# Optimization experiments

Hardware: AMD Instinct MI355X
Metric: run time of the kernel (lower is better)

The kernel has to match this reference:

```python
import jax, jax.numpy as jnp
import numpy as np

N_NODES = 10000
N_EDGES = 50000
NUM_GENES = 1000
HEADS = 8
DIMS_IN = [256, 448 * 8, 384 * 8, 256 * 8]
DIMS_OUT = [448, 384, 256, NUM_GENES]
HEADS_L = [8, 8, 8, 1]


def _leaky_relu(x):
    return jnp.where(x >= 0, x, 0.2 * x)


def gat_conv(x, src, dst, n, W, a_src, a_dst, b, heads, c):
    # W: [heads*c, f_in]; a_src/a_dst: [heads, c]; b: [heads*c]
    h = (x @ W.T).reshape(n, heads, c)                      # [N,H,C]
    al_s = jnp.einsum('nhc,hc->nh', h, a_src)               # [N,H]
    al_d = jnp.einsum('nhc,hc->nh', h, a_dst)
    e = _leaky_relu(al_s[src] + al_d[dst])                  # [E,H]
    # segment softmax over incoming edges of each dst node
    m = jax.ops.segment_max(e, dst, num_segments=n)
    e = jnp.exp(e - m[dst])
    s = jax.ops.segment_sum(e, dst, num_segments=n)
    alpha = e / (s[dst] + 1e-16)
    out = jax.ops.segment_sum(h[src] * alpha[:, :, None], dst, num_segments=n)
    return out.reshape(n, heads * c) + b


def graph_ln(x, w, b):
    # PyG LayerNorm mode='graph': normalize over all node features of the graph
    mu = x.mean()
    var = ((x - mu) ** 2).mean()
    return (x - mu) * jax.lax.rsqrt(var + 1e-5) * w + b


def setup_inputs() -> dict:
    key = jax.random.key(0)
    ks = jax.random.split(key, 32)
    inp = {
        'x': jax.random.normal(ks[0], (N_NODES, DIMS_IN[0]), dtype=jnp.float32),
        'edge_index': jax.random.randint(ks[1], (2, N_EDGES), 0, N_NODES, dtype=jnp.int32),
    }
    ki = 2
    for li in range(4):
        h, c, fin = HEADS_L[li], DIMS_OUT[li], DIMS_IN[li]
        inp[f'W{li+1}'] = jax.random.normal(ks[ki], (h * c, fin), dtype=jnp.float32) * (fin ** -0.5); ki += 1
        inp[f'a_src{li+1}'] = jax.random.normal(ks[ki], (h, c), dtype=jnp.float32) * 0.1; ki += 1
        inp[f'a_dst{li+1}'] = jax.random.normal(ks[ki], (h, c), dtype=jnp.float32) * 0.1; ki += 1
        inp[f'b{li+1}'] = jnp.zeros((h * c,), dtype=jnp.float32)
        if li < 3:
            inp[f'ln{li+1}_w'] = jnp.ones((h * c,), dtype=jnp.float32)
            inp[f'ln{li+1}_b'] = jnp.zeros((h * c,), dtype=jnp.float32)
    return inp


def reference(x, edge_index,
              W1, a_src1, a_dst1, b1, ln1_w, ln1_b,
              W2, a_src2, a_dst2, b2, ln2_w, ln2_b,
              W3, a_src3, a_dst3, b3, ln3_w, ln3_b,
              W4, a_src4, a_dst4, b4):
    n = x.shape[0]
    loops = jnp.arange(n, dtype=edge_index.dtype)
    src = jnp.concatenate([edge_index[0], loops])  # add_self_loops=True (PyG default)
    dst = jnp.concatenate([edge_index[1], loops])
    h = jax.nn.relu(gat_conv(x, src, dst, n, W1, a_src1, a_dst1, b1, 8, 448))
    h = graph_ln(h, ln1_w, ln1_b)
    h = jax.nn.relu(gat_conv(h, src, dst, n, W2, a_src2, a_dst2, b2, 8, 384))
    h = graph_ln(h, ln2_w, ln2_b)
    h = jax.nn.relu(gat_conv(h, src, dst, n, W3, a_src3, a_dst3, b3, 8, 256))
    h = graph_ln(h, ln3_w, ln3_b)
    out = gat_conv(h, src, dst, n, W4, a_src4, a_dst4, b4, 1, NUM_GENES)
    return out
```

## Files before the change

kernel.cpp:

```cpp
#include <hip/hip_runtime.h>

typedef _Float16 h8 __attribute__((ext_vector_type(8)));
typedef _Float16 h4 __attribute__((ext_vector_type(4)));
typedef __attribute__((ext_vector_type(4))) float facc4;

__device__ __forceinline__ void gload16(const void* g, void* l) {
  __builtin_amdgcn_global_load_lds((const __attribute__((address_space(1))) void*)g,
                                   (__attribute__((address_space(3))) void*)l, 16, 0, 0);
}

__global__ void f2h_k(const float* __restrict__ in, unsigned short* __restrict__ out, int n4) {
  int i = blockIdx.x * 256 + threadIdx.x;
  int stride = gridDim.x * 256;
  for (; i < n4; i += stride) {
    float4 v = ((const float4*)in)[i];
    h4 o;
    o[0] = (_Float16)v.x; o[1] = (_Float16)v.y; o[2] = (_Float16)v.z; o[3] = (_Float16)v.w;
    ((h4*)out)[i] = o;
  }
}

__global__ __launch_bounds__(512, 2) void gemm_f16(
    const unsigned short* __restrict__ A, const unsigned short* __restrict__ B,
    unsigned short* __restrict__ Hout,
    float* __restrict__ als, float* __restrict__ ald,
    const float* __restrict__ a_src, const float* __restrict__ a_dst,
    int M, int Nn, int K, int C, int H, int gx, int nwg) {
  __shared__ unsigned short lds[3 * 24576];
  const int tid = threadIdx.x, lane = tid & 63, wv = tid >> 6;

  int lin = blockIdx.x;
  int q = nwg >> 3, r = nwg & 7;
  int xcd = lin & 7, idx = lin >> 3;
  int swz = (xcd < r) ? (xcd * (q + 1) + idx) : (r * (q + 1) + (xcd - r) * q + idx);
  const int bx = swz % gx, by = swz / gx;
  const int brow = by * 256, bcol = bx * 128;
  const int wr = wv >> 1, wc = wv & 1;

  const int lr = lane >> 3;
  const int gslot = (lane & 7) ^ lr;
  const unsigned short* pa[4]; int ldsA[4];
#pragma unroll
  for (int i = 0; i < 4; ++i) {
    int rl = wv * 32 + i * 8 + lr;
    int rg = brow + rl; if (rg > M - 1) rg = M - 1;
    pa[i] = A + (size_t)rg * K + gslot * 8;
    ldsA[i] = (wv * 32 + i * 8) * 64;
  }
  const unsigned short* pb[2]; int ldsB[2];
#pragma unroll
  for (int i = 0; i < 2; ++i) {
    int rl = wv * 16 + i * 8 + lr;
    int rg = bcol + rl; if (rg > Nn - 1) rg = Nn - 1;
    pb[i] = B + (size_t)rg * K + gslot * 8;
    ldsB[i] = 16384 + (wv * 16 + i * 8) * 64;
  }

  const int ra0 = wr * 64 + (lane & 15);
  const int rb0 = wc * 64 + (lane & 15);
  const int g16 = lane >> 4;
  const int lx = lane & 7;

  facc4 acc[4][4] = {};
  const int nt = K >> 6;

  auto STAGE = [&](int kt, int buf) {
    const int bo = buf * 24576;
#pragma unroll
    for (int i = 0; i < 4; ++i) gload16(pa[i] + kt * 64, &lds[bo + ldsA[i]]);
#pragma unroll
    for (int i = 0; i < 2; ++i) gload16(pb[i] + kt * 64, &lds[bo + ldsB[i]]);
  };

  STAGE(0, 0);
  STAGE(1, 1);
  asm volatile("s_waitcnt vmcnt(6)" ::: "memory");
  __builtin_amdgcn_s_barrier();
  asm volatile("" ::: "memory");

  int cb = 0, sb = 2;
  for (int kt = 0; kt < nt; ++kt) {
    if (kt + 2 < nt) STAGE(kt + 2, sb);
    const int bo = cb * 24576;
#pragma unroll
    for (int kk = 0; kk < 2; ++kk) {
      const int slot = (kk * 4 + g16) ^ lx;
      h8 af[4], bf[4];
#pragma unroll
      for (int i = 0; i < 4; ++i) af[i] = *(const h8*)&lds[bo + (ra0 + i * 16) * 64 + slot * 8];
#pragma unroll
      for (int j = 0; j < 4; ++j) bf[j] = *(const h8*)&lds[bo + 16384 + (rb0 + j * 16) * 64 + slot * 8];
      __builtin_amdgcn_s_setprio(1);
#pragma unroll
      for (int i = 0; i < 4; ++i)
#pragma unroll
        for (int j = 0; j < 4; ++j)
          acc[i][j] = __builtin_amdgcn_mfma_f32_16x16x32_f16(af[i], bf[j], acc[i][j], 0, 0, 0);
      __builtin_amdgcn_s_setprio(0);
    }
    if (kt + 2 < nt) asm volatile("s_waitcnt vmcnt(6)" ::: "memory");
    else             asm volatile("s_waitcnt vmcnt(0)" ::: "memory");
    __builtin_amdgcn_s_barrier();
    asm volatile("" ::: "memory");
    cb = (cb == 2) ? 0 : cb + 1;
    sb = (sb == 2) ? 0 : sb + 1;
  }

  const int rbase = brow + wr * 64 + ((lane >> 4) << 2);
  const int cbase = bcol + wc * 64 + (lane & 15);

  float asv[4], adv[4];
#pragma unroll
  for (int j = 0; j < 4; ++j) {
    int col = cbase + j * 16;
    bool ok = col < Nn;
    asv[j] = ok ? a_src[col] : 0.f;
    adv[j] = ok ? a_dst[col] : 0.f;
  }
  const int hh = (bcol + wc * 64) / C;
#pragma unroll
  for (int i = 0; i < 4; ++i)
#pragma unroll
    for (int r2 = 0; r2 < 4; ++r2) {
      float s1 = 0.f, s2 = 0.f;
#pragma unroll
      for (int j = 0; j < 4; ++j) { float v = acc[i][j][r2]; s1 += v * asv[j]; s2 += v * adv[j]; }
#pragma unroll
      for (int m = 1; m < 16; m <<= 1) { s1 += __shfl_xor(s1, m); s2 += __shfl_xor(s2, m); }
      int row = rbase + i * 16 + r2;
      if ((lane & 15) == 0 && row < M) {
        atomicAdd(&als[row * H + hh], s1);
        atomicAdd(&ald[row * H + hh], s2);
      }
    }

#pragma unroll
  for (int i = 0; i < 4; ++i)
#pragma unroll
    for (int j = 0; j < 4; ++j) {
      int col = cbase + j * 16;
      if (col >= Nn) continue;
#pragma unroll
      for (int r2 = 0; r2 < 4; ++r2) {
        int row = rbase + i * 16 + r2;
        if (row < M) {
          _Float16 hv = (_Float16)acc[i][j][r2];
          Hout[(size_t)row * Nn + col] = *(unsigned short*)&hv;
        }
      }
    }
}

__global__ void count_deg_k(const int* __restrict__ ei, int* __restrict__ deg, int Ereal, int Etot) {
  int e = blockIdx.x * 256 + threadIdx.x;
  if (e >= Etot) return;
  int dst = (e < Ereal) ? ei[Ereal + e] : (e - Ereal);
  atomicAdd(&deg[dst], 1);
}

__global__ void scan_k(const int* __restrict__ deg, int* __restrict__ rowptr, int n) {
  __shared__ int sums[1024];
  int t = threadIdx.x;
  int base = t * 10;
  int loc[10]; int s = 0;
#pragma unroll
  for (int i = 0; i < 10; ++i) { int idx = base + i; int d = (idx < n) ? deg[idx] : 0; loc[i] = s; s += d; }
  sums[t] = s;
  __syncthreads();
  for (int off = 1; off < 1024; off <<= 1) {
    int add = (t >= off) ? sums[t - off] : 0;
    __syncthreads();
    sums[t] += add;
    __syncthreads();
  }
  int excl = sums[t] - s;
#pragma unroll
  for (int i = 0; i < 10; ++i) { int idx = base + i; if (idx < n) rowptr[idx] = excl + loc[i]; }
  if (t == 1023) rowptr[n] = sums[1023];
}

__global__ void scatter_k(const int* __restrict__ ei, const int* __restrict__ rowptr,
                          int* __restrict__ fill, int* __restrict__ esrc,
                          int Ereal, int Etot) {
  int e = blockIdx.x * 256 + threadIdx.x;
  if (e >= Etot) return;
  int src = (e < Ereal) ? ei[e] : (e - Ereal);
  int dst = (e < Ereal) ? ei[Ereal + e] : (e - Ereal);
  int pos = rowptr[dst] + atomicAdd(&fill[dst], 1);
  esrc[pos] = src;
}

template <int H, bool FP32OUT, bool STATS>
__global__ __launch_bounds__(256) void aggregate_k(
    const unsigned short* __restrict__ hfp,
    const float* __restrict__ als, const float* __restrict__ ald,
    const int* __restrict__ rowptr, const int* __restrict__ esrc,
    const float* __restrict__ bias, void* __restrict__ outv,
    float* __restrict__ lnsums, int C, int F) {
  const int node = blockIdx.x;
  const int tid = threadIdx.x;
  int beg = rowptr[node];
  int deg = rowptr[node + 1] - beg;
  if (deg > 128) deg = 128;
  __shared__ int   s_src[128];
  __shared__ float s_p[128][H];
  __shared__ float s_inv[H];
  float aldv[H];
#pragma unroll
  for (int h = 0; h < H; ++h) aldv[h] = ald[node * H + h];
  for (int d = tid; d < deg; d += 256) {
    int s = esrc[beg + d];
    s_src[d] = s;
#pragma unroll
    for (int h = 0; h < H; ++h) {
      float v = als[s * H + h] + aldv[h];
      s_p[d][h] = (v >= 0.f) ? v : 0.2f * v;
    }
  }
  __syncthreads();
  if (tid < H) {
    float m = -1e30f;
    for (int d = 0; d < deg; ++d) m = fmaxf(m, s_p[d][tid]);
    float s = 0.f;
    for (int d = 0; d < deg; ++d) { float p = __expf(s_p[d][tid] - m); s_p[d][tid] = p; s += p; }
    s_inv[tid] = 1.f / (s + 1e-16f);
  }
  __syncthreads();

  float s1 = 0.f, s2 = 0.f;
  const int F8 = F >> 3;
  for (int c8 = tid; c8 < F8; c8 += 256) {
    int f0 = c8 * 8;
    int h = f0 / C;
    float a[8];
    float4 b0 = *(const float4*)(bias + f0);
    float4 b1 = *(const float4*)(bias + f0 + 4);
    a[0] = b0.x; a[1] = b0.y; a[2] = b0.z; a[3] = b0.w;
    a[4] = b1.x; a[5] = b1.y; a[6] = b1.z; a[7] = b1.w;
    for (int d = 0; d < deg; ++d) {
      float al = s_p[d][h] * s_inv[h];
      h8 hv = *(const h8*)(hfp + (size_t)s_src[d] * F + f0);
#pragma unroll
      for (int j = 0; j < 8; ++j) a[j] = fmaf(al, (float)hv[j], a[j]);
    }
    size_t i = (size_t)node * F + f0;
    if (FP32OUT) {
      float4 o0 = {a[0], a[1], a[2], a[3]};
      float4 o1 = {a[4], a[5], a[6], a[7]};
      *(float4*)((float*)outv + i) = o0;
      *(float4*)((float*)outv + i + 4) = o1;
    } else {
      h8 o;
#pragma unroll
      for (int j = 0; j < 8; ++j) o[j] = (_Float16)a[j];
      *(h8*)((unsigned short*)outv + i) = o;
    }
    if (STATS) {
#pragma unroll
      for (int j = 0; j < 8; ++j) { float v = a[j] > 0.f ? a[j] : 0.f; s1 += v; s2 += v * v; }
    }
  }
  if (STATS) {
#pragma unroll
    for (int m = 32; m; m >>= 1) { s1 += __shfl_down(s1, m); s2 += __shfl_down(s2, m); }
    __shared__ float r1[4], r2[4];
    if ((tid & 63) == 0) { r1[tid >> 6] = s1; r2[tid >> 6] = s2; }
    __syncthreads();
    if (tid == 0) {
      atomicAdd(&lnsums[0], r1[0] + r1[1] + r1[2] + r1[3]);
      atomicAdd(&lnsums[1], r2[0] + r2[1] + r2[2] + r2[3]);
    }
  }
}

__global__ void ln_apply_k(unsigned short* __restrict__ x, const float* __restrict__ sums,
                           const float* __restrict__ w, const float* __restrict__ b,
                           int total8, int F8, float inv_count) {
  int i8 = blockIdx.x * 256 + threadIdx.x;
  if (i8 >= total8) return;
  float mu = sums[0] * inv_count;
  float var = sums[1] * inv_count - mu * mu;
  float istd = rsqrtf(var + 1e-5f);
  int f0 = (i8 % F8) * 8;
  h8 hv = *(h8*)(x + (size_t)i8 * 8);
  float4 w0 = *(const float4*)(w + f0), w1 = *(const float4*)(w + f0 + 4);
  float4 b0 = *(const float4*)(b + f0), b1 = *(const float4*)(b + f0 + 4);
  float wv[8] = {w0.x, w0.y, w0.z, w0.w, w1.x, w1.y, w1.z, w1.w};
  float bv[8] = {b0.x, b0.y, b0.z, b0.w, b1.x, b1.y, b1.z, b1.w};
  h8 o;
#pragma unroll
  for (int j = 0; j < 8; ++j) {
    float v = (float)hv[j]; v = v > 0.f ? v : 0.f;
    o[j] = (_Float16)((v - mu) * istd * wv[j] + bv[j]);
  }
  *(h8*)(x + (size_t)i8 * 8) = o;
}

extern "C" void kernel_launch(void* const* d_in, const int* in_sizes, int n_in,
                              void* d_out, int out_size, void* d_ws, size_t ws_size,
                              hipStream_t stream) {
  const int N = 10000, Ereal = 50000, Etot = 60000;
  const float* x  = (const float*)d_in[0];
  const int*   ei = (const int*)d_in[1];
  const float* W[4]    = {(const float*)d_in[2],  (const float*)d_in[8],  (const float*)d_in[14], (const float*)d_in[20]};
  const float* asrc[4] = {(const float*)d_in[3],  (const float*)d_in[9],  (const float*)d_in[15], (const float*)d_in[21]};
  const float* adst[4] = {(const float*)d_in[4],  (const float*)d_in[10], (const float*)d_in[16], (const float*)d_in[22]};
  const float* bias[4] = {(const float*)d_in[5],  (const float*)d_in[11], (const float*)d_in[17], (const float*)d_in[23]};
  const float* lnw[3]  = {(const float*)d_in[6],  (const float*)d_in[12], (const float*)d_in[18]};
  const float* lnb[3]  = {(const float*)d_in[7],  (const float*)d_in[13], (const float*)d_in[19]};

  const int fin[4]  = {256, 3584, 3072, 2048};
  const int fout[4] = {3584, 3072, 2048, 1000};
  const int CH[4]   = {448, 384, 256, 1000};

  size_t off = 0;
  char* base = (char*)d_ws;
  auto alloc = [&](size_t bytes) -> void* {
    void* p = base + off;
    off += (bytes + 255) & ~(size_t)255;
    return p;
  };
  unsigned short* xh  = (unsigned short*)alloc((size_t)N * 3584 * 2);
  unsigned short* hh  = (unsigned short*)alloc((size_t)N * 3584 * 2);
  unsigned short* wh  = (unsigned short*)alloc((size_t)3072 * 3584 * 2);
  float*          als    = (float*)alloc((size_t)N * 8 * 4);
  float*          ald    = (float*)alloc((size_t)N * 8 * 4);
  int*            deg    = (int*)alloc((size_t)N * 4);
  int*            fill   = (int*)alloc((size_t)N * 4);
  int*            rowptr = (int*)alloc((size_t)(N + 1) * 4);
  int*            esrc   = (int*)alloc((size_t)Etot * 4);
  float*          lnsums = (float*)alloc(256);

  auto cdiv = [](int a, int b) { return (a + b - 1) / b; };

  hipMemsetAsync(deg, 0, (size_t)N * 4, stream);
  hipMemsetAsync(fill, 0, (size_t)N * 4, stream);
  count_deg_k<<<cdiv(Etot, 256), 256, 0, stream>>>(ei, deg, Ereal, Etot);
  scan_k<<<1, 1024, 0, stream>>>(deg, rowptr, N);
  scatter_k<<<cdiv(Etot, 256), 256, 0, stream>>>(ei, rowptr, fill, esrc, Ereal, Etot);

  {
    int n4 = (N * fin[0]) / 4;
    f2h_k<<<min(2048, cdiv(n4, 256)), 256, 0, stream>>>(x, xh, n4);
  }

  for (int l = 0; l < 4; ++l) {
    const int K = fin[l], Fo = fout[l], C = CH[l];
    const int H = (l == 3) ? 1 : 8;

    {
      int n4 = (Fo * K) / 4;
      f2h_k<<<min(2048, cdiv(n4, 256)), 256, 0, stream>>>(W[l], wh, n4);
    }

    hipMemsetAsync(als, 0, (size_t)N * 8 * 4 * 2, stream);

    {
      int gx = cdiv(Fo, 128), gy = cdiv(N, 256);
      int nwg = gx * gy;
      gemm_f16<<<nwg, 512, 0, stream>>>(xh, wh, hh, als, ald, asrc[l], adst[l],
                                        N, Fo, K, C, H, gx, nwg);
    }

    if (l < 3) {
      hipMemsetAsync(lnsums, 0, 8, stream);
      aggregate_k<8, false, true><<<N, 256, 0, stream>>>(hh, als, ald, rowptr, esrc,
                                                         bias[l], xh, lnsums, C, Fo);
      int F8 = Fo >> 3;
      int total8 = N * F8;
      ln_apply_k<<<cdiv(total8, 256), 256, 0, stream>>>(xh, lnsums, lnw[l], lnb[l],
                                                        total8, F8, 1.0f / (float)(N * Fo));
    } else {
      aggregate_k<1, true, false><<<N, 256, 0, stream>>>(hh, als, ald, rowptr, esrc,
                                                         bias[l], d_out, nullptr, C, Fo);
    }
  }
}
```

Baseline: 1.577 ms.

## Enlarge GEMM tile to 256x256 with BK=32 and hoist logit memsets

The fused GEMM kernel's output tile grows from 256x128 to 256x256. Each of the 8 waves now computes a 128x64 sub-tile, and the K step shrinks from 64 to 32 with a new XOR-swizzled LDS layout, aiming for more reuse of A and B per byte loaded. The attention-logit buffers become one slice per layer, cleared by a single up-front memset instead of one memset per layer. The trade-off is a much larger register footprint per wave (128 accumulator floats plus 48 registers of fragments) under the existing 512-thread, 2-block launch bound, which risks spills. It also launches fewer workgroups for the narrower layers.

Measured after the change: 1.629 ms. +3.3%, slower.

```diff
diff --git a/kernel.cpp b/kernel.cpp
--- a/kernel.cpp
+++ b/kernel.cpp
@@ -26,7 +26,7 @@
     float* __restrict__ als, float* __restrict__ ald,
     const float* __restrict__ a_src, const float* __restrict__ a_dst,
     int M, int Nn, int K, int C, int H, int gx, int nwg) {
-  __shared__ unsigned short lds[3 * 24576];
+  __shared__ __align__(16) unsigned short lds[3 * 16384];
   const int tid = threadIdx.x, lane = tid & 63, wv = tid >> 6;
 
   int lin = blockIdx.x;
@@ -34,71 +34,60 @@
   int xcd = lin & 7, idx = lin >> 3;
   int swz = (xcd < r) ? (xcd * (q + 1) + idx) : (r * (q + 1) + (xcd - r) * q + idx);
   const int bx = swz % gx, by = swz / gx;
-  const int brow = by * 256, bcol = bx * 128;
-  const int wr = wv >> 1, wc = wv & 1;
-
-  const int lr = lane >> 3;
-  const int gslot = (lane & 7) ^ lr;
-  const unsigned short* pa[4]; int ldsA[4];
-#pragma unroll
-  for (int i = 0; i < 4; ++i) {
-    int rl = wv * 32 + i * 8 + lr;
-    int rg = brow + rl; if (rg > M - 1) rg = M - 1;
-    pa[i] = A + (size_t)rg * K + gslot * 8;
-    ldsA[i] = (wv * 32 + i * 8) * 64;
-  }
-  const unsigned short* pb[2]; int ldsB[2];
-#pragma unroll
-  for (int i = 0; i < 2; ++i) {
-    int rl = wv * 16 + i * 8 + lr;
-    int rg = bcol + rl; if (rg > Nn - 1) rg = Nn - 1;
-    pb[i] = B + (size_t)rg * K + gslot * 8;
-    ldsB[i] = 16384 + (wv * 16 + i * 8) * 64;
-  }
-
-  const int ra0 = wr * 64 + (lane & 15);
-  const int rb0 = wc * 64 + (lane & 15);
-  const int g16 = lane >> 4;
-  const int lx = lane & 7;
-
-  facc4 acc[4][4] = {};
-  const int nt = K >> 6;
+  const int brow = by * 256, bcol = bx * 256;
+  const int wr = wv >> 2, wc = wv & 3;
+
+  const int l4 = lane >> 2;
+  const int srcslot = ((lane & 3) ^ ((lane >> 3) & 3)) * 8;
+  int ar0 = brow + wv * 16 + l4;        if (ar0 > M - 1)  ar0 = M - 1;
+  int ar1 = brow + wv * 16 + 128 + l4;  if (ar1 > M - 1)  ar1 = M - 1;
+  int br0 = bcol + wv * 16 + l4;        if (br0 > Nn - 1) br0 = Nn - 1;
+  int br1 = bcol + wv * 16 + 128 + l4;  if (br1 > Nn - 1) br1 = Nn - 1;
+  const unsigned short* pa0 = A + (size_t)ar0 * K + srcslot;
+  const unsigned short* pa1 = A + (size_t)ar1 * K + srcslot;
+  const unsigned short* pb0 = B + (size_t)br0 * K + srcslot;
+  const unsigned short* pb1 = B + (size_t)br1 * K + srcslot;
+  const int d0 = wv * 512, d1 = wv * 512 + 4096;
+
+  const int rsl = ((lane >> 4) ^ (((lane & 15) >> 1) & 3)) * 8;
+  const int baseA = (wr * 128 + (lane & 15)) * 32 + rsl;
+  const int baseB = 8192 + (wc * 64 + (lane & 15)) * 32 + rsl;
+
+  facc4 acc[8][4] = {};
+  const int nt = K >> 5;
 
   auto STAGE = [&](int kt, int buf) {
-    const int bo = buf * 24576;
-#pragma unroll
-    for (int i = 0; i < 4; ++i) gload16(pa[i] + kt * 64, &lds[bo + ldsA[i]]);
-#pragma unroll
-    for (int i = 0; i < 2; ++i) gload16(pb[i] + kt * 64, &lds[bo + ldsB[i]]);
+    unsigned short* Lq = &lds[buf * 16384];
+    const int kb = kt * 32;
+    gload16(pa0 + kb, Lq + d0);
+    gload16(pa1 + kb, Lq + d1);
+    gload16(pb0 + kb, Lq + 8192 + d0);
+    gload16(pb1 + kb, Lq + 8192 + d1);
   };
 
   STAGE(0, 0);
   STAGE(1, 1);
-  asm volatile("s_waitcnt vmcnt(6)" ::: "memory");
+  asm volatile("s_waitcnt vmcnt(4)" ::: "memory");
   __builtin_amdgcn_s_barrier();
   asm volatile("" ::: "memory");
 
   int cb = 0, sb = 2;
   for (int kt = 0; kt < nt; ++kt) {
     if (kt + 2 < nt) STAGE(kt + 2, sb);
-    const int bo = cb * 24576;
-#pragma unroll
-    for (int kk = 0; kk < 2; ++kk) {
-      const int slot = (kk * 4 + g16) ^ lx;
-      h8 af[4], bf[4];
-#pragma unroll
-      for (int i = 0; i < 4; ++i) af[i] = *(const h8*)&lds[bo + (ra0 + i * 16) * 64 + slot * 8];
-#pragma unroll
-      for (int j = 0; j < 4; ++j) bf[j] = *(const h8*)&lds[bo + 16384 + (rb0 + j * 16) * 64 + slot * 8];
-      __builtin_amdgcn_s_setprio(1);
-#pragma unroll
-      for (int i = 0; i < 4; ++i)
-#pragma unroll
-        for (int j = 0; j < 4; ++j)
-          acc[i][j] = __builtin_amdgcn_mfma_f32_16x16x32_f16(af[i], bf[j], acc[i][j], 0, 0, 0);
-      __builtin_amdgcn_s_setprio(0);
-    }
-    if (kt + 2 < nt) asm volatile("s_waitcnt vmcnt(6)" ::: "memory");
+    const unsigned short* Lq = &lds[cb * 16384];
+    h8 af[8], bf[4];
+#pragma unroll
+    for (int m = 0; m < 8; ++m) af[m] = *(const h8*)(Lq + baseA + m * 512);
+#pragma unroll
+    for (int n = 0; n < 4; ++n) bf[n] = *(const h8*)(Lq + baseB + n * 512);
+    __builtin_amdgcn_s_setprio(1);
+#pragma unroll
+    for (int m = 0; m < 8; ++m)
+#pragma unroll
+      for (int n = 0; n < 4; ++n)
+        acc[m][n] = __builtin_amdgcn_mfma_f32_16x16x32_f16(af[m], bf[n], acc[m][n], 0, 0, 0);
+    __builtin_amdgcn_s_setprio(0);
+    if (kt + 2 < nt) asm volatile("s_waitcnt vmcnt(4)" ::: "memory");
     else             asm volatile("s_waitcnt vmcnt(0)" ::: "memory");
     __builtin_amdgcn_s_barrier();
     asm volatile("" ::: "memory");
@@ -106,28 +95,28 @@
     sb = (sb == 2) ? 0 : sb + 1;
   }
 
-  const int rbase = brow + wr * 64 + ((lane >> 4) << 2);
+  const int rbase = brow + wr * 128 + ((lane >> 4) << 2);
   const int cbase = bcol + wc * 64 + (lane & 15);
 
   float asv[4], adv[4];
 #pragma unroll
-  for (int j = 0; j < 4; ++j) {
-    int col = cbase + j * 16;
+  for (int n = 0; n < 4; ++n) {
+    int col = cbase + n * 16;
     bool ok = col < Nn;
-    asv[j] = ok ? a_src[col] : 0.f;
-    adv[j] = ok ? a_dst[col] : 0.f;
+    asv[n] = ok ? a_src[col] : 0.f;
+    adv[n] = ok ? a_dst[col] : 0.f;
   }
   const int hh = (bcol + wc * 64) / C;
 #pragma unroll
-  for (int i = 0; i < 4; ++i)
+  for (int m = 0; m < 8; ++m)
 #pragma unroll
     for (int r2 = 0; r2 < 4; ++r2) {
       float s1 = 0.f, s2 = 0.f;
 #pragma unroll
-      for (int j = 0; j < 4; ++j) { float v = acc[i][j][r2]; s1 += v * asv[j]; s2 += v * adv[j]; }
-#pragma unroll
-      for (int m = 1; m < 16; m <<= 1) { s1 += __shfl_xor(s1, m); s2 += __shfl_xor(s2, m); }
-      int row = rbase + i * 16 + r2;
+      for (int n = 0; n < 4; ++n) { float v = acc[m][n][r2]; s1 += v * asv[n]; s2 += v * adv[n]; }
+#pragma unroll
+      for (int mm = 1; mm < 16; mm <<= 1) { s1 += __shfl_xor(s1, mm); s2 += __shfl_xor(s2, mm); }
+      int row = rbase + m * 16 + r2;
       if ((lane & 15) == 0 && row < M) {
         atomicAdd(&als[row * H + hh], s1);
         atomicAdd(&ald[row * H + hh], s2);
@@ -135,16 +124,16 @@
     }
 
 #pragma unroll
-  for (int i = 0; i < 4; ++i)
-#pragma unroll
-    for (int j = 0; j < 4; ++j) {
-      int col = cbase + j * 16;
+  for (int m = 0; m < 8; ++m)
+#pragma unroll
+    for (int n = 0; n < 4; ++n) {
+      int col = cbase + n * 16;
       if (col >= Nn) continue;
 #pragma unroll
       for (int r2 = 0; r2 < 4; ++r2) {
-        int row = rbase + i * 16 + r2;
+        int row = rbase + m * 16 + r2;
         if (row < M) {
-          _Float16 hv = (_Float16)acc[i][j][r2];
+          _Float16 hv = (_Float16)acc[m][n][r2];
           Hout[(size_t)row * Nn + col] = *(unsigned short*)&hv;
         }
       }
@@ -323,8 +312,8 @@
   unsigned short* xh  = (unsigned short*)alloc((size_t)N * 3584 * 2);
   unsigned short* hh  = (unsigned short*)alloc((size_t)N * 3584 * 2);
   unsigned short* wh  = (unsigned short*)alloc((size_t)3072 * 3584 * 2);
-  float*          als    = (float*)alloc((size_t)N * 8 * 4);
-  float*          ald    = (float*)alloc((size_t)N * 8 * 4);
+  float*          alsA   = (float*)alloc((size_t)4 * N * 8 * 4);
+  float*          aldA   = (float*)alloc((size_t)4 * N * 8 * 4);
   int*            deg    = (int*)alloc((size_t)N * 4);
   int*            fill   = (int*)alloc((size_t)N * 4);
   int*            rowptr = (int*)alloc((size_t)(N + 1) * 4);
@@ -335,6 +324,7 @@
 
   hipMemsetAsync(deg, 0, (size_t)N * 4, stream);
   hipMemsetAsync(fill, 0, (size_t)N * 4, stream);
+  hipMemsetAsync(alsA, 0, (size_t)4 * N * 8 * 4 * 2, stream);
   count_deg_k<<<cdiv(Etot, 256), 256, 0, stream>>>(ei, deg, Ereal, Etot);
   scan_k<<<1, 1024, 0, stream>>>(deg, rowptr, N);
   scatter_k<<<cdiv(Etot, 256), 256, 0, stream>>>(ei, rowptr, fill, esrc, Ereal, Etot);
@@ -347,16 +337,16 @@
   for (int l = 0; l < 4; ++l) {
     const int K = fin[l], Fo = fout[l], C = CH[l];
     const int H = (l == 3) ? 1 : 8;
+    float* als = alsA + (size_t)l * N * 8;
+    float* ald = aldA + (size_t)l * N * 8;
 
     {
       int n4 = (Fo * K) / 4;
       f2h_k<<<min(2048, cdiv(n4, 256)), 256, 0, stream>>>(W[l], wh, n4);
     }
 
-    hipMemsetAsync(als, 0, (size_t)N * 8 * 4 * 2, stream);
-
     {
-      int gx = cdiv(Fo, 128), gy = cdiv(N, 256);
+      int gx = cdiv(Fo, 256), gy = cdiv(N, 256);
       int nwg = gx * gy;
       gemm_f16<<<nwg, 512, 0, stream>>>(xh, wh, hh, als, ald, asrc[l], adst[l],
                                         N, Fo, K, C, H, gx, nwg);
```
